# Kernel tuning notes

Hardware: AMD Instinct MI355X
Metric: run time of the kernel (lower is better)

The kernel has to match this reference:

```python
import jax, jax.numpy as jnp
import numpy as np

B, L, D, H = 8, 1024, 768, 12
HD = D // H
EPS = 1e-5
R_EPS = 1e-12  # numerical guard for r at coincident positions


def setup_inputs() -> dict:
    key = jax.random.key(0)
    ks = jax.random.split(key, 8)
    x = jax.random.normal(ks[0], (B, L, D), dtype=jnp.float32)
    # 32x32 patch grid coordinates, same for every batch element
    g = jnp.arange(32, dtype=jnp.float32)
    yy, xx = jnp.meshgrid(g, g, indexing='ij')
    pos = jnp.broadcast_to(jnp.stack([yy.ravel(), xx.ravel()], axis=-1), (B, L, 2))
    w_norm = jnp.ones((D,), dtype=jnp.float32)
    w_in = 0.02 * jax.random.normal(ks[1], (3 * D, D), dtype=jnp.float32)
    b_in = jnp.zeros((3 * D,), dtype=jnp.float32)
    w_out = 0.02 * jax.random.normal(ks[2], (D, D), dtype=jnp.float32)
    b_out = jnp.zeros((D,), dtype=jnp.float32)
    # bias params [H, 6] = (o, c, w, p, delta, m) per init_bias_params
    o = jnp.zeros((H,), dtype=jnp.float32)
    c = 1.0 + 0.3 * jax.random.uniform(ks[3], (H,), dtype=jnp.float32)
    w = jnp.ones((H,), dtype=jnp.float32)
    p = jnp.zeros((H,), dtype=jnp.float32)
    delta = jax.random.normal(ks[4], (H,), dtype=jnp.float32)
    m = jnp.ones((H,), dtype=jnp.float32)
    bias_params = jnp.stack([o, c, w, p, delta, m], axis=-1)
    return {"x": x, "pos": pos, "w_norm": w_norm, "w_in": w_in, "b_in": b_in,
            "w_out": w_out, "b_out": b_out, "bias_params": bias_params}


def _bias_grid(pos, bias_params):
    # pos: [B, L, 2] -> bias: [B, H, L, L]
    o, c, w, p, delta, m = [bias_params[:, i].reshape(1, H, 1, 1) for i in range(6)]
    dist = pos[:, :, None, :] - pos[:, None, :, :]          # [B, Lq, Lk, 2]
    theta = jnp.arctan2(dist[..., 1], dist[..., 0])[:, None]  # [B, 1, Lq, Lk]
    r = jnp.sqrt(jnp.sum(dist * dist, axis=-1) + R_EPS)[:, None]
    term1 = jax.nn.relu(r - o) ** jnp.abs(c)
    term2 = 1.0 - jnp.abs(jnp.tanh(delta)) * (jnp.cos((theta - p) * w * 0.5) ** 2) ** jnp.abs(m)
    return term1 * term2


def reference(x, pos, w_norm, w_in, b_in, w_out, b_out, bias_params):
    bias = _bias_grid(pos, bias_params)                      # [B, H, L, L]
    # RMSNorm
    xn = x * jax.lax.rsqrt(jnp.mean(x * x, axis=-1, keepdims=True) + EPS) * w_norm
    qkv = xn @ w_in.T + b_in                                 # [B, L, 3D]
    q, k, v = jnp.split(qkv, 3, axis=-1)
    def heads(t):
        return t.reshape(B, L, H, HD).transpose(0, 2, 1, 3)  # [B, H, L, HD]
    q, k, v = heads(q), heads(k), heads(v)
    scores = jnp.einsum('bhqd,bhkd->bhqk', q, k) / jnp.sqrt(jnp.float32(HD)) + bias
    attn = jax.nn.softmax(scores, axis=-1)
    o = jnp.einsum('bhqk,bhkd->bhqd', attn, v)
    o = o.transpose(0, 2, 1, 3).reshape(B, L, D)
    return o @ w_out.T + b_out
```

## Files before the change

kernel.cpp:

```cpp
#include <hip/hip_runtime.h>

#define BB 8
#define LL 1024
#define DD 768
#define HH 12
#define HD 64

typedef short s16x8 __attribute__((ext_vector_type(8)));
typedef float f32x4 __attribute__((ext_vector_type(4)));
typedef unsigned int u32x4 __attribute__((ext_vector_type(4)));

static __device__ __forceinline__ unsigned short f2bf(float f){
  unsigned int u = __builtin_bit_cast(unsigned int, f);
  u = (u + 0x7FFFu + ((u >> 16) & 1u)) >> 16;
  return (unsigned short)u;
}

static __device__ __forceinline__ unsigned int cvtpk_bf(float a, float b){
  unsigned int r;
  asm("v_cvt_pk_bf16_f32 %0, %1, %2" : "=v"(r) : "v"(a), "v"(b));
  return r;
}

static __device__ __forceinline__ void swap32(unsigned int& a, unsigned int& b){
  asm("v_permlane32_swap_b32 %0, %1" : "+v"(a), "+v"(b));
}
static __device__ __forceinline__ void swap16(unsigned int& a, unsigned int& b){
  asm("v_permlane16_swap_b32 %0, %1" : "+v"(a), "+v"(b));
}

static __device__ __forceinline__ float hexp2(float x){
#if __has_builtin(__builtin_amdgcn_exp2f)
  return __builtin_amdgcn_exp2f(x);
#else
  return exp2f(x);
#endif
}

static __device__ __forceinline__ f32x4 mfma16(s16x8 a, s16x8 b, f32x4 c){
  return __builtin_amdgcn_mfma_f32_16x16x32_bf16(a, b, c, 0, 0, 0);
}

static __device__ __forceinline__ void gld_lds16(const void* g, void* l){
  __builtin_amdgcn_global_load_lds(
      (const __attribute__((address_space(1))) void*)g,
      (__attribute__((address_space(3))) void*)l, 16, 0, 0);
}

__global__ void cvt_kernel(const float* __restrict__ src, unsigned short* __restrict__ dst, int n4){
  int i = blockIdx.x*256 + threadIdx.x;
  if (i < n4){
    float4 v = ((const float4*)src)[i];
    ushort4 o;
    o.x = f2bf(v.x); o.y = f2bf(v.y); o.z = f2bf(v.z); o.w = f2bf(v.w);
    ((ushort4*)dst)[i] = o;
  }
}

__global__ void bias_table_kernel(const float* __restrict__ bp, float* __restrict__ table){
  int idx = blockIdx.x*256 + threadIdx.x;
  if (idx >= HH*3969) return;
  int hh = idx/3969, rem = idx - hh*3969;
  int dy = rem/63 - 31, dx = rem%63 - 31;
  float o  = bp[hh*6+0], c = bp[hh*6+1], w = bp[hh*6+2];
  float p  = bp[hh*6+3], dl = bp[hh*6+4], m = bp[hh*6+5];
  float theta = atan2f((float)dx, (float)dy);
  float r = sqrtf((float)(dy*dy + dx*dx) + 1e-12f);
  float t1 = powf(fmaxf(r - o, 0.0f), fabsf(c));
  float co = cosf((theta - p)*w*0.5f);
  float t2 = 1.0f - fabsf(tanhf(dl))*powf(co*co, fabsf(m));
  table[idx] = t1*t2*1.44269504f;
}

__global__ __launch_bounds__(64) void bmax_kernel(const float* __restrict__ table,
                                                  float* __restrict__ bmax){
  int qy = blockIdx.x, h = blockIdx.y;
  __shared__ float m1[63];
  int t = threadIdx.x;
  const float* tb = table + h*3969;
  if (t < 63){
    float m = -3.0e38f;
    #pragma unroll 4
    for (int row = qy; row < qy + 32; row++) m = fmaxf(m, tb[row*63 + t]);
    m1[t] = m;
  }
  __syncthreads();
  if (t < 32){
    float m = -3.0e38f;
    #pragma unroll 4
    for (int c = t; c < t + 32; c++) m = fmaxf(m, m1[c]);
    bmax[(h*32 + qy)*32 + t] = m;
  }
}

__global__ __launch_bounds__(256) void rmsnorm_kernel(const float* __restrict__ x,
                                                      const float* __restrict__ wn,
                                                      unsigned short* __restrict__ xn){
  int row = blockIdx.x, t = threadIdx.x;
  const float* xr = x + (size_t)row*DD;
  float v0 = xr[t], v1 = xr[t+256], v2 = xr[t+512];
  float ss = v0*v0 + v1*v1 + v2*v2;
  #pragma unroll
  for (int m = 1; m < 64; m <<= 1) ss += __shfl_xor(ss, m, 64);
  __shared__ float red[4];
  if ((t & 63) == 0) red[t >> 6] = ss;
  __syncthreads();
  float tot = red[0] + red[1] + red[2] + red[3];
  float sc = rsqrtf(tot*(1.0f/DD) + 1e-5f);
  unsigned short* xo = xn + (size_t)row*DD;
  xo[t]     = f2bf(v0*sc*wn[t]);
  xo[t+256] = f2bf(v1*sc*wn[t+256]);
  xo[t+512] = f2bf(v2*sc*wn[t+512]);
}

static __device__ __forceinline__ void storeC(float* p, float v){ *p = v; }
static __device__ __forceinline__ void storeC(unsigned short* p, float v){ *p = f2bf(v); }

template<int MODE, int TN, typename OutT>
__global__ __launch_bounds__(256) void gemm_bt_kernel(const unsigned short* __restrict__ A,
                                                      const unsigned short* __restrict__ B,
                                                      const float* __restrict__ bias,
                                                      OutT* __restrict__ C,
                                                      unsigned short* __restrict__ qp,
                                                      unsigned short* __restrict__ kp,
                                                      unsigned short* __restrict__ vp,
                                                      int M, int N, int K){
  constexpr int NT = TN/32;
  constexpr int SMEM_BYTES = 192*(128 + TN);
  __shared__ __align__(16) char smem[SMEM_BYTES];
  unsigned short* As = (unsigned short*)smem;
  unsigned short* Bs = (unsigned short*)(smem + 3*128*32*2);
  int tid = threadIdx.x;
  int w = tid >> 6, lane = tid & 63, quad = lane >> 4, col = lane & 15;
  int wm = (w >> 1)*64, wn = (w & 1)*(TN/2);
  int bm = blockIdx.x*128, bn = blockIdx.y*TN;

  int srow = lane >> 2;
  int schunk = (lane & 3)*8;
  const unsigned short* ga0 = A + (size_t)(bm + w*32 + srow)*K + schunk;
  const unsigned short* ga1 = ga0 + (size_t)16*K;
  const unsigned short* gb0 = B + (size_t)(bn + w*(TN/4) + srow)*K + schunk;
  const unsigned short* gb1 = gb0 + (size_t)16*K;

  auto stage = [&](int t, int bi){
    int kk = t*32;
    gld_lds16(ga0 + kk, As + bi*4096 + (w*32)*32);
    gld_lds16(ga1 + kk, As + bi*4096 + (w*32 + 16)*32);
    gld_lds16(gb0 + kk, Bs + bi*(TN*32) + (w*(TN/4))*32);
    if (TN == 128) gld_lds16(gb1 + kk, Bs + bi*(TN*32) + (w*32 + 16)*32);
  };

  f32x4 acc[4][NT];
  #pragma unroll
  for (int mt = 0; mt < 4; mt++)
    #pragma unroll
    for (int nt = 0; nt < NT; nt++) acc[mt][nt] = (f32x4){0.f,0.f,0.f,0.f};

  stage(0, 0);
  stage(1, 1);

  int KT = K >> 5;
  int buf = 0, nbuf = 2;
  for (int t = 0; t < KT; t++){
    if (t < KT - 1){
      if (TN == 128) asm volatile("s_waitcnt vmcnt(4)" ::: "memory");
      else           asm volatile("s_waitcnt vmcnt(3)" ::: "memory");
    } else {
      asm volatile("s_waitcnt vmcnt(0)" ::: "memory");
    }
    __builtin_amdgcn_s_barrier();
    asm volatile("" ::: "memory");
    if (t + 2 < KT) stage(t + 2, nbuf);
    s16x8 af[4], bfr[NT];
    #pragma unroll
    for (int mt = 0; mt < 4; mt++)
      af[mt] = *(const s16x8*)&As[buf*4096 + (wm + mt*16 + col)*32 + quad*8];
    #pragma unroll
    for (int nt = 0; nt < NT; nt++)
      bfr[nt] = *(const s16x8*)&Bs[buf*(TN*32) + (wn + nt*16 + col)*32 + quad*8];
    #pragma unroll
    for (int mt = 0; mt < 4; mt++)
      #pragma unroll
      for (int nt = 0; nt < NT; nt++)
        acc[mt][nt] = mfma16(af[mt], bfr[nt], acc[mt][nt]);
    buf  = (buf  == 2) ? 0 : buf  + 1;
    nbuf = (nbuf == 2) ? 0 : nbuf + 1;
  }

  if (MODE == 1){
    __syncthreads();
    unsigned short* Ct = (unsigned short*)smem;
    #pragma unroll
    for (int mt = 0; mt < 4; mt++)
      #pragma unroll
      for (int nt = 0; nt < NT; nt++){
        int cc = wn + nt*16 + col;
        float bv = bias[bn + cc];
        #pragma unroll
        for (int r = 0; r < 4; r++){
          int row = wm + mt*16 + quad*4 + r;
          Ct[row*136 + cc] = f2bf(acc[mt][nt][r] + bv);
        }
      }
    __syncthreads();
    #pragma unroll
    for (int e = 0; e < 8; e++){
      int id = e*256 + tid;
      int row = id >> 4, ch = id & 15;
      s16x8 val = *(const s16x8*)&Ct[row*136 + ch*8];
      int rw = bm + row;
      int cl0 = bn + ch*8;
      int part = cl0 >= 1536 ? 2 : (cl0 >= 768 ? 1 : 0);
      int hd = cl0 - part*768;
      int hh2 = hd >> 6, d0 = hd & 63;
      int bb = rw >> 10, l = rw & 1023;
      size_t base = (((size_t)bb*HH + hh2)*LL + l)*64;
      if (part == 0)      *(s16x8*)(qp + base + d0) = val;
      else if (part == 1) *(s16x8*)(kp + base + (((d0>>3) ^ (l&7)) << 3)) = val;
      else                *(s16x8*)(vp + base + d0) = val;
    }
  } else {
    #pragma unroll
    for (int mt = 0; mt < 4; mt++)
      #pragma unroll
      for (int nt = 0; nt < NT; nt++){
        int cl = bn + wn + nt*16 + col;
        float bv = bias[cl];
        #pragma unroll
        for (int r = 0; r < 4; r++){
          int rw = bm + wm + mt*16 + quad*4 + r;
          storeC(&C[(size_t)rw*N + cl], acc[mt][nt][r] + bv);
        }
      }
  }
}

__global__ __launch_bounds__(256) void vtrans_kernel(const unsigned short* __restrict__ vp,
                                                     unsigned short* __restrict__ vt2){
  int jt = blockIdx.x, bh = blockIdx.y;
  __shared__ unsigned short tile[32][68];
  int t = threadIdx.x;
  const unsigned short* src = vp + ((size_t)bh*LL + jt*32)*64;
  #pragma unroll
  for (int e = 0; e < 8; e++){
    int lin = t + 256*e;
    tile[lin >> 6][lin & 63] = src[lin];
  }
  __syncthreads();
  unsigned short* dst = vt2 + ((size_t)bh*32 + jt)*2048;
  #pragma unroll
  for (int e = 0; e < 8; e++){
    int lin = t + 256*e;
    dst[lin] = tile[lin & 31][lin >> 5];
  }
}

__global__ __launch_bounds__(128) void attn_kernel(const unsigned short* __restrict__ qp,
                                                   const unsigned short* __restrict__ kp,
                                                   const unsigned short* __restrict__ vt2,
                                                   const float* __restrict__ table,
                                                   const float* __restrict__ bmax,
                                                   const float* __restrict__ pos,
                                                   unsigned short* __restrict__ o_out){
  int i = blockIdx.x;
  int bh = (i >> 7)*8 + (i & 7);
  int qt = (i >> 3) & 7;
  int wp = (i >> 6) & 1;
  int b = bh/HH, h = bh - b*HH;
  int tid = threadIdx.x, w = tid >> 6, lane = tid & 63, quad = lane >> 4, col = lane & 15;
  __shared__ float tl[3969];

  const unsigned short* kgp = kp  + (size_t)bh*65536;
  const unsigned short* vgp = vt2 + (size_t)bh*65536;

  int sw = col & 7;
  int k_r0 = col*64 + ((quad ^ sw) << 3);
  int k_r1 = col*64 + (((quad + 4) ^ sw) << 3);
  int v_r  = col*32 + quad*8;

  s16x8 kA[4], vA[4], kB[4], vB[4];
  auto issue = [&](int t, s16x8 (&k)[4], s16x8 (&v)[4]){
    const unsigned short* kt = kgp + t*2048;
    const unsigned short* vt = vgp + t*2048;
    k[0] = *(const s16x8*)(kt + k_r0);
    k[1] = *(const s16x8*)(kt + k_r1);
    k[2] = *(const s16x8*)(kt + 1024 + k_r0);
    k[3] = *(const s16x8*)(kt + 1024 + k_r1);
    v[0] = *(const s16x8*)(vt + v_r);
    v[1] = *(const s16x8*)(vt + v_r + 512);
    v[2] = *(const s16x8*)(vt + v_r + 1024);
    v[3] = *(const s16x8*)(vt + v_r + 1536);
  };
  issue(0, kA, vA);
  issue(1, kB, vB);

  for (int j = tid; j < 3969; j += 128) tl[j] = table[h*3969 + j];
  const float* pb = pos + (size_t)b*2048;

  int qw = qt*128 + (wp*2 + w)*32;
  const unsigned short* qpb = qp + (size_t)bh*65536;
  s16x8 qa[2][2];
  int cq[2];
  f32x4 zb[2];
  #pragma unroll
  for (int g = 0; g < 2; g++){
    int q = qw + g*16 + col;
    size_t qo = (size_t)q*64 + quad*8;
    qa[g][0] = *(const s16x8*)(qpb + qo);
    qa[g][1] = *(const s16x8*)(qpb + qo + 32);
    int qy = __float2int_rn(pb[q*2]);
    int qx = __float2int_rn(pb[q*2 + 1]);
    cq[g] = qy*63 + qx + 1984 - quad*4;
    float neg = -5.5451774445f * bmax[(h*32 + qy)*32 + qx];
    zb[g] = (f32x4){neg, neg, neg, neg};
  }

  s16x8 ones;
  #pragma unroll
  for (int e = 0; e < 8; e++) ones[e] = (short)0x3F80;

  f32x4 o[2][4];
  f32x4 l_acc[2];
  #pragma unroll
  for (int g = 0; g < 2; g++){
    #pragma unroll
    for (int nt = 0; nt < 4; nt++) o[g][nt] = (f32x4){0.f,0.f,0.f,0.f};
    l_acc[g] = (f32x4){0.f,0.f,0.f,0.f};
  }

  __syncthreads();

  auto step = [&](int t, s16x8 (&k)[4], s16x8 (&v)[4]){
    int kyt = 63*t;
    #pragma unroll
    for (int g = 0; g < 2; g++){
      f32x4 s_lo = mfma16(k[0], qa[g][0], zb[g]);  s_lo = mfma16(k[1], qa[g][1], s_lo);
      f32x4 s_hi = mfma16(k[2], qa[g][0], zb[g]);  s_hi = mfma16(k[3], qa[g][1], s_hi);
      int base = cq[g] - kyt;
      float pl[4], ph[4];
      #pragma unroll
      for (int r = 0; r < 4; r++){
        pl[r] = hexp2(__builtin_fmaf(s_lo[r], 0.18033688f, tl[base - r]));
        ph[r] = hexp2(__builtin_fmaf(s_hi[r], 0.18033688f, tl[base - r - 16]));
      }
      unsigned int wA = cvtpk_bf(pl[0], pl[1]);
      unsigned int wB = cvtpk_bf(pl[2], pl[3]);
      unsigned int wC = cvtpk_bf(ph[0], ph[1]);
      unsigned int wD = cvtpk_bf(ph[2], ph[3]);
      swap32(wA, wC);  swap32(wB, wD);
      swap16(wA, wC);  swap16(wB, wD);
      u32x4 pv4; pv4.x = wA; pv4.y = wB; pv4.z = wC; pv4.w = wD;
      s16x8 pf = __builtin_bit_cast(s16x8, pv4);
      l_acc[g] = mfma16(ones, pf, l_acc[g]);
      o[g][0] = mfma16(v[0], pf, o[g][0]);
      o[g][1] = mfma16(v[1], pf, o[g][1]);
      o[g][2] = mfma16(v[2], pf, o[g][2]);
      o[g][3] = mfma16(v[3], pf, o[g][3]);
    }
  };

  for (int t = 0; t < 32; t += 2){
    step(t, kA, vA);
    if (t + 2 < 32) issue(t + 2, kA, vA);
    step(t + 1, kB, vB);
    if (t + 3 < 32) issue(t + 3, kB, vB);
  }

  #pragma unroll
  for (int g = 0; g < 2; g++){
    float inv = 1.0f / l_acc[g][0];
    int q = qw + g*16 + col;
    unsigned short* orow = o_out + (size_t)(b*LL + q)*DD + h*64;
    #pragma unroll
    for (int nt = 0; nt < 4; nt++){
      uint2 pkd;
      pkd.x = cvtpk_bf(o[g][nt][0]*inv, o[g][nt][1]*inv);
      pkd.y = cvtpk_bf(o[g][nt][2]*inv, o[g][nt][3]*inv);
      *(uint2*)&orow[nt*16 + quad*4] = pkd;
    }
  }
}

extern "C" void kernel_launch(void* const* d_in, const int* in_sizes, int n_in,
                              void* d_out, int out_size, void* d_ws, size_t ws_size,
                              hipStream_t stream){
  const float* x      = (const float*)d_in[0];
  const float* pos    = (const float*)d_in[1];
  const float* w_norm = (const float*)d_in[2];
  const float* w_in   = (const float*)d_in[3];
  const float* b_in   = (const float*)d_in[4];
  const float* w_out  = (const float*)d_in[5];
  const float* b_out  = (const float*)d_in[6];
  const float* bp     = (const float*)d_in[7];

  char* ws = (char*)d_ws;
  unsigned short* xn    = (unsigned short*)(ws);
  unsigned short* winb  = (unsigned short*)(ws + 12582912);
  unsigned short* woutb = (unsigned short*)(ws + 16121856);
  unsigned short* qpb   = (unsigned short*)(ws + 17301504);
  unsigned short* kpb   = (unsigned short*)(ws + 29884416);
  unsigned short* vpb   = (unsigned short*)(ws + 42467328);
  unsigned short* vt2b  = (unsigned short*)(ws + 55050240);
  float*          table = (float*)        (ws + 67633152);
  unsigned short* ob    = (unsigned short*)(ws + 67823664);
  float*          bmaxp = (float*)        (ws);

  cvt_kernel<<<dim3((2304*768/4)/256), dim3(256), 0, stream>>>(w_in, winb, 2304*768/4);
  cvt_kernel<<<dim3((768*768/4)/256), dim3(256), 0, stream>>>(w_out, woutb, 768*768/4);
  bias_table_kernel<<<dim3((HH*3969 + 255)/256), dim3(256), 0, stream>>>(bp, table);
  rmsnorm_kernel<<<dim3(BB*LL), dim3(256), 0, stream>>>(x, w_norm, xn);
  gemm_bt_kernel<1, 128, unsigned short><<<dim3(64, 18), dim3(256), 0, stream>>>(
      xn, winb, b_in, (unsigned short*)nullptr, qpb, kpb, vpb, BB*LL, 3*DD, DD);
  bmax_kernel<<<dim3(32, HH), dim3(64), 0, stream>>>(table, bmaxp);
  vtrans_kernel<<<dim3(32, BB*HH), dim3(256), 0, stream>>>(vpb, vt2b);
  attn_kernel<<<dim3(1536), dim3(128), 0, stream>>>(qpb, kpb, vt2b, table, bmaxp, pos, ob);
  gemm_bt_kernel<0, 64, float><<<dim3(64, 12), dim3(256), 0, stream>>>(
      ob, woutb, b_out, (float*)d_out, nullptr, nullptr, nullptr, BB*LL, DD, DD);
}
```

Baseline: 227.1 us.

## Fuse prep kernels, swizzle GEMM LDS tiles, stage output stores, prioritize MFMA

Merges the two weight-conversion kernels and the bias-table kernel into one launch. It XOR-swizzles the GEMM LDS chunk layout on both load and read to cut bank conflicts. The fp32 output GEMM epilogue is staged through LDS so global stores are coalesced float4 writes. s_setprio is raised around MFMA groups in attention to favour matrix issue. Each change adds some risk: extra barriers in the epilogue, swizzle correctness, and scheduling effects of the priority hints.

```diff
diff --git a/kernel.cpp b/kernel.cpp
--- a/kernel.cpp
+++ b/kernel.cpp
@@ -47,29 +47,39 @@
       (__attribute__((address_space(3))) void*)l, 16, 0, 0);
 }
 
-__global__ void cvt_kernel(const float* __restrict__ src, unsigned short* __restrict__ dst, int n4){
-  int i = blockIdx.x*256 + threadIdx.x;
-  if (i < n4){
-    float4 v = ((const float4*)src)[i];
+__global__ __launch_bounds__(256) void prep_kernel(const float* __restrict__ w_in,
+                                                   unsigned short* __restrict__ winb,
+                                                   const float* __restrict__ w_out,
+                                                   unsigned short* __restrict__ woutb,
+                                                   const float* __restrict__ bp,
+                                                   float* __restrict__ table){
+  int bid = blockIdx.x, tid = threadIdx.x;
+  if (bid < 1728){
+    int i = bid*256 + tid;
+    float4 v = ((const float4*)w_in)[i];
     ushort4 o;
     o.x = f2bf(v.x); o.y = f2bf(v.y); o.z = f2bf(v.z); o.w = f2bf(v.w);
-    ((ushort4*)dst)[i] = o;
-  }
-}
-
-__global__ void bias_table_kernel(const float* __restrict__ bp, float* __restrict__ table){
-  int idx = blockIdx.x*256 + threadIdx.x;
-  if (idx >= HH*3969) return;
-  int hh = idx/3969, rem = idx - hh*3969;
-  int dy = rem/63 - 31, dx = rem%63 - 31;
-  float o  = bp[hh*6+0], c = bp[hh*6+1], w = bp[hh*6+2];
-  float p  = bp[hh*6+3], dl = bp[hh*6+4], m = bp[hh*6+5];
-  float theta = atan2f((float)dx, (float)dy);
-  float r = sqrtf((float)(dy*dy + dx*dx) + 1e-12f);
-  float t1 = powf(fmaxf(r - o, 0.0f), fabsf(c));
-  float co = cosf((theta - p)*w*0.5f);
-  float t2 = 1.0f - fabsf(tanhf(dl))*powf(co*co, fabsf(m));
-  table[idx] = t1*t2*1.44269504f;
+    ((ushort4*)winb)[i] = o;
+  } else if (bid < 2304){
+    int i = (bid - 1728)*256 + tid;
+    float4 v = ((const float4*)w_out)[i];
+    ushort4 o;
+    o.x = f2bf(v.x); o.y = f2bf(v.y); o.z = f2bf(v.z); o.w = f2bf(v.w);
+    ((ushort4*)woutb)[i] = o;
+  } else {
+    int idx = (bid - 2304)*256 + tid;
+    if (idx >= HH*3969) return;
+    int hh = idx/3969, rem = idx - hh*3969;
+    int dy = rem/63 - 31, dx = rem%63 - 31;
+    float o  = bp[hh*6+0], c = bp[hh*6+1], w = bp[hh*6+2];
+    float p  = bp[hh*6+3], dl = bp[hh*6+4], m = bp[hh*6+5];
+    float theta = atan2f((float)dx, (float)dy);
+    float r = sqrtf((float)(dy*dy + dx*dx) + 1e-12f);
+    float t1 = powf(fmaxf(r - o, 0.0f), fabsf(c));
+    float co = cosf((theta - p)*w*0.5f);
+    float t2 = 1.0f - fabsf(tanhf(dl))*powf(co*co, fabsf(m));
+    table[idx] = t1*t2*1.44269504f;
+  }
 }
 
 __global__ __launch_bounds__(64) void bmax_kernel(const float* __restrict__ table,
@@ -136,7 +146,7 @@
   int bm = blockIdx.x*128, bn = blockIdx.y*TN;
 
   int srow = lane >> 2;
-  int schunk = (lane & 3)*8;
+  int schunk = (((lane & 3) ^ ((lane >> 3) & 3)))*8;
   const unsigned short* ga0 = A + (size_t)(bm + w*32 + srow)*K + schunk;
   const unsigned short* ga1 = ga0 + (size_t)16*K;
   const unsigned short* gb0 = B + (size_t)(bn + w*(TN/4) + srow)*K + schunk;
@@ -158,6 +168,9 @@
 
   stage(0, 0);
   stage(1, 1);
+
+  int rsw = (col >> 1) & 3;
+  int rchunk = (quad ^ rsw)*8;
 
   int KT = K >> 5;
   int buf = 0, nbuf = 2;
@@ -174,10 +187,10 @@
     s16x8 af[4], bfr[NT];
     #pragma unroll
     for (int mt = 0; mt < 4; mt++)
-      af[mt] = *(const s16x8*)&As[buf*4096 + (wm + mt*16 + col)*32 + quad*8];
+      af[mt] = *(const s16x8*)&As[buf*4096 + (wm + mt*16 + col)*32 + rchunk];
     #pragma unroll
     for (int nt = 0; nt < NT; nt++)
-      bfr[nt] = *(const s16x8*)&Bs[buf*(TN*32) + (wn + nt*16 + col)*32 + quad*8];
+      bfr[nt] = *(const s16x8*)&Bs[buf*(TN*32) + (wn + nt*16 + col)*32 + rchunk];
     #pragma unroll
     for (int mt = 0; mt < 4; mt++)
       #pragma unroll
@@ -220,18 +233,28 @@
       else                *(s16x8*)(vp + base + d0) = val;
     }
   } else {
+    __syncthreads();
+    float* Cf = (float*)smem;
     #pragma unroll
     for (int mt = 0; mt < 4; mt++)
       #pragma unroll
       for (int nt = 0; nt < NT; nt++){
-        int cl = bn + wn + nt*16 + col;
-        float bv = bias[cl];
+        int cc = wn + nt*16 + col;
+        float bv = bias[bn + cc];
         #pragma unroll
         for (int r = 0; r < 4; r++){
-          int rw = bm + wm + mt*16 + quad*4 + r;
-          storeC(&C[(size_t)rw*N + cl], acc[mt][nt][r] + bv);
+          int row = wm + mt*16 + quad*4 + r;
+          Cf[row*68 + cc] = acc[mt][nt][r] + bv;
         }
       }
+    __syncthreads();
+    #pragma unroll
+    for (int e = 0; e < 8; e++){
+      int id = e*256 + tid;
+      int row = id >> 4, ch = id & 15;
+      float4 val = *(const float4*)&Cf[row*68 + ch*4];
+      *(float4*)&C[(size_t)(bm + row)*N + bn + ch*4] = val;
+    }
   }
 }
 
@@ -334,8 +357,10 @@
     int kyt = 63*t;
     #pragma unroll
     for (int g = 0; g < 2; g++){
+      __builtin_amdgcn_s_setprio(1);
       f32x4 s_lo = mfma16(k[0], qa[g][0], zb[g]);  s_lo = mfma16(k[1], qa[g][1], s_lo);
       f32x4 s_hi = mfma16(k[2], qa[g][0], zb[g]);  s_hi = mfma16(k[3], qa[g][1], s_hi);
+      __builtin_amdgcn_s_setprio(0);
       int base = cq[g] - kyt;
       float pl[4], ph[4];
       #pragma unroll
@@ -351,11 +376,13 @@
       swap16(wA, wC);  swap16(wB, wD);
       u32x4 pv4; pv4.x = wA; pv4.y = wB; pv4.z = wC; pv4.w = wD;
       s16x8 pf = __builtin_bit_cast(s16x8, pv4);
+      __builtin_amdgcn_s_setprio(1);
       l_acc[g] = mfma16(ones, pf, l_acc[g]);
       o[g][0] = mfma16(v[0], pf, o[g][0]);
       o[g][1] = mfma16(v[1], pf, o[g][1]);
       o[g][2] = mfma16(v[2], pf, o[g][2]);
       o[g][3] = mfma16(v[3], pf, o[g][3]);
+      __builtin_amdgcn_s_setprio(0);
     }
   };
 
@@ -405,9 +432,7 @@
   unsigned short* ob    = (unsigned short*)(ws + 67823664);
   float*          bmaxp = (float*)        (ws);
 
-  cvt_kernel<<<dim3((2304*768/4)/256), dim3(256), 0, stream>>>(w_in, winb, 2304*768/4);
-  cvt_kernel<<<dim3((768*768/4)/256), dim3(256), 0, stream>>>(w_out, woutb, 768*768/4);
-  bias_table_kernel<<<dim3((HH*3969 + 255)/256), dim3(256), 0, stream>>>(bp, table);
+  prep_kernel<<<dim3(2491), dim3(256), 0, stream>>>(w_in, winb, w_out, woutb, bp, table);
   rmsnorm_kernel<<<dim3(BB*LL), dim3(256), 0, stream>>>(x, w_norm, xn);
   gemm_bt_kernel<1, 128, unsigned short><<<dim3(64, 18), dim3(256), 0, stream>>>(
       xn, winb, b_in, (unsigned short*)nullptr, qpb, kpb, vpb, BB*LL, 3*DD, DD);
```

New measurement: 224.7 us. No clear change (-1.1%).
